# Optimization experiments

Hardware: AMD Instinct MI355X
Metric: run time of the kernel (lower is better)

## Reference

```python
import jax, jax.numpy as jnp
import numpy as np

N_Q = 32   # query window / partition increment
N_K = 128  # key window length
H = 8      # heads


def _ln(x, w=None, b=None, eps=1e-5):
    m = jnp.mean(x, axis=-1, keepdims=True)
    v = jnp.var(x, axis=-1, keepdims=True)
    y = (x - m) * jax.lax.rsqrt(v + eps)
    if w is not None:
        y = y * w
    if b is not None:
        y = y + b
    return y


def setup_inputs() -> dict:
    key = jax.random.key(0)
    ks = jax.random.split(key, 16)
    B, N, C, CP = 1, 2048, 128, 16
    sc = 1.0 / np.sqrt(C)
    inp = {
        "x": jax.random.normal(ks[0], (B, N, C), jnp.float32),
        "s": jax.random.normal(ks[1], (B, N, C), jnp.float32),
        "pair": jax.random.normal(ks[2], (B, N, N, CP), jnp.float32),
        "adaln_s_w": jnp.ones((C,), jnp.float32),
        "adaln_gate_w": jax.random.normal(ks[3], (C, C), jnp.float32) * sc,
        "adaln_gate_b": jnp.zeros((C,), jnp.float32),
        "adaln_skip_w": jax.random.normal(ks[4], (C, C), jnp.float32) * sc,
        "q_w": jax.random.normal(ks[5], (C, C), jnp.float32) * sc,
        "q_b": jnp.zeros((C,), jnp.float32),
        "k_w": jax.random.normal(ks[6], (C, C), jnp.float32) * sc,
        "v_w": jax.random.normal(ks[7], (C, C), jnp.float32) * sc,
        "pair_ln_w": jnp.ones((CP,), jnp.float32),
        "pair_ln_b": jnp.zeros((CP,), jnp.float32),
        "pair_proj_w": jax.random.normal(ks[8], (CP, H), jnp.float32) * 0.25,
        "gate_w": jax.random.normal(ks[9], (C, C), jnp.float32) * sc,
        "attn_proj_w": jax.random.normal(ks[10], (C, C), jnp.float32) * sc,
        "out_w": jax.random.normal(ks[11], (C, C), jnp.float32) * sc,
        "out_b": jnp.full((C,), -2.0, jnp.float32),
    }
    return inp


def reference(x, s, pair, adaln_s_w, adaln_gate_w, adaln_gate_b, adaln_skip_w,
              q_w, q_b, k_w, v_w, pair_ln_w, pair_ln_b, pair_proj_w,
              gate_w, attn_proj_w, out_w, out_b):
    B, N, C = x.shape
    nb = N // N_Q          # number of local blocks
    pad = (N_K - N_Q) // 2  # 48: zero halo on each side
    hd = C // H

    # AdaLN: LN(a) no affine; LN(s) scale-only; gate + skip from s
    a = _ln(x)
    sn = _ln(s, adaln_s_w)
    a = jax.nn.sigmoid(sn @ adaln_gate_w + adaln_gate_b) * a + sn @ adaln_skip_w

    q = a @ q_w + q_b
    k = a @ k_w
    v = a @ v_w

    # local windows: window i covers padded[32i : 32i+128]
    idx = N_Q * jnp.arange(nb)[:, None] + jnp.arange(N_K)[None, :]  # [nb, N_K]

    def window(t):  # [B,N,C] -> [B,nb,N_K,C] with zero-padded edges
        tp = jnp.pad(t, ((0, 0), (pad, pad), (0, 0)))
        return tp[:, idx]

    qb = q.reshape(B, nb, N_Q, H, hd).transpose(0, 3, 1, 2, 4)        # [B,H,nb,NQ,hd]
    kb = window(k).reshape(B, nb, N_K, H, hd).transpose(0, 3, 1, 2, 4)
    vb = window(v).reshape(B, nb, N_K, H, hd).transpose(0, 3, 1, 2, 4)

    # pair bias -> local blocks [B,H,nb,NQ,NK]
    pb = _ln(pair, pair_ln_w, pair_ln_b) @ pair_proj_w                # [B,N,N,H]
    pb = pb.reshape(B, nb, N_Q, N, H)
    pb = jnp.pad(pb, ((0, 0), (0, 0), (0, 0), (pad, pad), (0, 0)))
    pb = jnp.take_along_axis(pb, idx[None, :, None, :, None], axis=3)  # [B,nb,NQ,NK,H]
    bias = pb.transpose(0, 4, 1, 2, 3)

    logits = jnp.einsum('bhnqd,bhnkd->bhnqk', qb, kb) / jnp.sqrt(jnp.float32(hd)) + bias
    attn = jax.nn.softmax(logits, axis=-1)
    o = jnp.einsum('bhnqk,bhnkd->bhnqd', attn, vb)
    o = o.transpose(0, 2, 3, 1, 4).reshape(B, N, C)

    g = jax.nn.sigmoid(o @ gate_w) * o
    out = g @ attn_proj_w
    out = jax.nn.sigmoid(out @ out_w + out_b) * out
    return out
```

## Files before the change

kernel.cpp:

```cpp
#include <hip/hip_runtime.h>
#include <math.h>

#define NTOK 2048
#define CDIM 128
#define HHEADS 8
#define HDIM 16
#define NQW 32
#define NKW 128
#define PADW 48
#define CPD 16
#define BT 8

__device__ __forceinline__ float sigmoid_(float z){ return 1.0f/(1.0f+__expf(-z)); }
__device__ __forceinline__ float rdlane(float v, int l){
    return __int_as_float(__builtin_amdgcn_readlane(__float_as_int(v), l));
}

__global__ __launch_bounds__(512, 4) void k_front(
    const float* __restrict__ x, const float* __restrict__ s,
    const float* __restrict__ s_w,
    const float* __restrict__ gate_w, const float* __restrict__ gate_b,
    const float* __restrict__ skip_w,
    const float* __restrict__ q_w, const float* __restrict__ q_b,
    const float* __restrict__ k_w, const float* __restrict__ v_w,
    const float* __restrict__ pair, const float* __restrict__ pln_w,
    const float* __restrict__ pln_b, const float* __restrict__ pproj,
    float* __restrict__ qo, float* __restrict__ ko, float* __restrict__ vo,
    float* __restrict__ bias)
{
    __shared__ float act_t[CDIM][10];
    __shared__ float sn_t[CDIM][10];
    __shared__ float part[8][2][BT][CDIM];
    const int tid = threadIdx.x;
    const int bid = blockIdx.x;

    if (bid >= NTOK/BT) {
        #pragma unroll
        for (int rep = 0; rep < 2; ++rep) {
            const int idx = (bid - NTOK/BT) * 1024 + rep*512 + tid;
            const int qg = idx >> 7;
            const int j  = idx & 127;
            const int ib = qg >> 5;
            const int qr = qg & 31;
            const int kg = (ib << 5) - PADW + j;
            float outh[HHEADS] = {0,0,0,0,0,0,0,0};
            if (kg >= 0 && kg < NTOK) {
                const float* p = pair + ((size_t)qg * NTOK + kg) * CPD;
                float buf[CPD];
                float sum = 0.f, ssq = 0.f;
                #pragma unroll
                for (int c = 0; c < CPD; c += 4) {
                    const float4 t4 = *(const float4*)(p + c);
                    buf[c+0]=t4.x; buf[c+1]=t4.y; buf[c+2]=t4.z; buf[c+3]=t4.w;
                    sum += t4.x+t4.y+t4.z+t4.w;
                    ssq += t4.x*t4.x+t4.y*t4.y+t4.z*t4.z+t4.w*t4.w;
                }
                const float m  = sum * (1.0f/CPD);
                const float vr = ssq * (1.0f/CPD) - m*m;
                const float rs = rsqrtf(vr + 1e-5f);
                #pragma unroll
                for (int c = 0; c < CPD; ++c) {
                    const float y = (buf[c]-m)*rs*pln_w[c] + pln_b[c];
                    #pragma unroll
                    for (int h = 0; h < HHEADS; ++h)
                        outh[h] = fmaf(y, pproj[c*HHEADS+h], outh[h]);
                }
            }
            float* bb = bias + ((size_t)(ib*HHEADS)*NQW + qr)*NKW + j;
            #pragma unroll
            for (int h = 0; h < HHEADS; ++h)
                bb[(size_t)h*NQW*NKW] = outh[h];
        }
        return;
    }

    const int tok0 = bid * BT;
    const int w = tid >> 6;
    const int L = tid & 63;

    {
        const float2 xv = *(const float2*)(x + (size_t)(tok0+w)*CDIM + 2*L);
        const float2 yv = *(const float2*)(s + (size_t)(tok0+w)*CDIM + 2*L);
        float sx = xv.x+xv.y, sxx = xv.x*xv.x+xv.y*xv.y;
        float sy = yv.x+yv.y, syy = yv.x*yv.x+yv.y*yv.y;
        #pragma unroll
        for (int m = 1; m < 64; m <<= 1) {
            sx  += __shfl_xor(sx,  m, 64);
            sxx += __shfl_xor(sxx, m, 64);
            sy  += __shfl_xor(sy,  m, 64);
            syy += __shfl_xor(syy, m, 64);
        }
        const float inv = 1.0f/128.0f;
        const float mx = sx*inv, vx = sxx*inv - mx*mx;
        const float my = sy*inv, vy = syy*inv - my*my;
        const float rx = rsqrtf(vx+1e-5f), ry = rsqrtf(vy+1e-5f);
        const float2 swv = *(const float2*)(s_w + 2*L);
        act_t[2*L][w]   = (xv.x-mx)*rx;
        act_t[2*L+1][w] = (xv.y-mx)*rx;
        sn_t[2*L][w]    = (yv.x-my)*ry*swv.x;
        sn_t[2*L+1][w]  = (yv.y-my)*ry*swv.y;
    }
    __syncthreads();

    const int i0 = w * 16;
    float snr0 = sn_t[i0 + (L>>3)][L&7];
    float snr1 = sn_t[i0 + 8 + (L>>3)][L&7];

    float ag[8][2] = {{0}}, as_[8][2] = {{0}};
    #pragma unroll
    for (int ii = 0; ii < 16; ++ii) {
        const float2 wg  = *(const float2*)(gate_w + (size_t)(i0+ii)*CDIM + 2*L);
        const float2 wsk = *(const float2*)(skip_w + (size_t)(i0+ii)*CDIM + 2*L);
        #pragma unroll
        for (int t = 0; t < 8; ++t) {
            const int v = ii*8 + t;
            const float a = rdlane((v < 64) ? snr0 : snr1, v & 63);
            ag[t][0]  = fmaf(a, wg.x,  ag[t][0]);
            ag[t][1]  = fmaf(a, wg.y,  ag[t][1]);
            as_[t][0] = fmaf(a, wsk.x, as_[t][0]);
            as_[t][1] = fmaf(a, wsk.y, as_[t][1]);
        }
    }
    #pragma unroll
    for (int t = 0; t < 8; ++t) {
        *(float2*)&part[w][0][t][2*L] = make_float2(ag[t][0],  ag[t][1]);
        *(float2*)&part[w][1][t][2*L] = make_float2(as_[t][0], as_[t][1]);
    }
    __syncthreads();

    const int j  = tid & 127;
    const int tq = tid >> 7;
    {
        float zg[2] = {0,0}, zs[2] = {0,0};
        #pragma unroll
        for (int ww = 0; ww < 8; ++ww) {
            #pragma unroll
            for (int tt = 0; tt < 2; ++tt) {
                zg[tt] += part[ww][0][2*tq+tt][j];
                zs[tt] += part[ww][1][2*tq+tt][j];
            }
        }
        const float gb = gate_b[j];
        const float2 av = *(const float2*)&act_t[j][2*tq];
        const float a2x = sigmoid_(zg[0]+gb)*av.x + zs[0];
        const float a2y = sigmoid_(zg[1]+gb)*av.y + zs[1];
        *(float2*)&sn_t[j][2*tq] = make_float2(a2x, a2y);
    }
    __syncthreads();

    float ar0 = sn_t[i0 + (L>>3)][L&7];
    float ar1 = sn_t[i0 + 8 + (L>>3)][L&7];
    float aq[8][2] = {{0}}, ak[8][2] = {{0}}, avv[8][2] = {{0}};
    #pragma unroll
    for (int ii = 0; ii < 16; ++ii) {
        const float2 wq = *(const float2*)(q_w + (size_t)(i0+ii)*CDIM + 2*L);
        const float2 wk = *(const float2*)(k_w + (size_t)(i0+ii)*CDIM + 2*L);
        const float2 wv = *(const float2*)(v_w + (size_t)(i0+ii)*CDIM + 2*L);
        #pragma unroll
        for (int t = 0; t < 8; ++t) {
            const int v = ii*8 + t;
            const float a = rdlane((v < 64) ? ar0 : ar1, v & 63);
            aq[t][0]  = fmaf(a, wq.x, aq[t][0]);
            aq[t][1]  = fmaf(a, wq.y, aq[t][1]);
            ak[t][0]  = fmaf(a, wk.x, ak[t][0]);
            ak[t][1]  = fmaf(a, wk.y, ak[t][1]);
            avv[t][0] = fmaf(a, wv.x, avv[t][0]);
            avv[t][1] = fmaf(a, wv.y, avv[t][1]);
        }
    }
    #pragma unroll
    for (int t = 0; t < 8; ++t) {
        *(float2*)&part[w][0][t][2*L] = make_float2(aq[t][0], aq[t][1]);
        *(float2*)&part[w][1][t][2*L] = make_float2(ak[t][0], ak[t][1]);
    }
    __syncthreads();
    {
        float zq[2] = {0,0}, zk[2] = {0,0};
        #pragma unroll
        for (int ww = 0; ww < 8; ++ww) {
            #pragma unroll
            for (int tt = 0; tt < 2; ++tt) {
                zq[tt] += part[ww][0][2*tq+tt][j];
                zk[tt] += part[ww][1][2*tq+tt][j];
            }
        }
        const float qbj = q_b[j];
        #pragma unroll
        for (int tt = 0; tt < 2; ++tt) {
            const size_t row = (size_t)(tok0 + 2*tq + tt)*CDIM + j;
            qo[row] = zq[tt] + qbj;
            ko[row] = zk[tt];
        }
    }
    __syncthreads();
    #pragma unroll
    for (int t = 0; t < 8; ++t)
        *(float2*)&part[w][0][t][2*L] = make_float2(avv[t][0], avv[t][1]);
    __syncthreads();
    {
        float zv[2] = {0,0};
        #pragma unroll
        for (int ww = 0; ww < 8; ++ww) {
            #pragma unroll
            for (int tt = 0; tt < 2; ++tt)
                zv[tt] += part[ww][0][2*tq+tt][j];
        }
        #pragma unroll
        for (int tt = 0; tt < 2; ++tt)
            vo[(size_t)(tok0 + 2*tq + tt)*CDIM + j] = zv[tt];
    }
}

__global__ __launch_bounds__(256) void k_attn(
    const float* __restrict__ qi, const float* __restrict__ ki,
    const float* __restrict__ vi, const float* __restrict__ bias,
    float* __restrict__ o)
{
    __shared__ float khs[NKW*20];
    __shared__ float vhs[NKW*20];
    const int ib = blockIdx.x;
    const int h  = blockIdx.y;
    const int t  = threadIdx.x;

    {
        const int jr  = t >> 1;
        const int d08 = (t & 1) * 8;
        const int kg  = ib*NQW - PADW + jr;
        float4 k0 = {0,0,0,0}, k1 = {0,0,0,0};
        float4 v0 = {0,0,0,0}, v1 = {0,0,0,0};
        if (kg >= 0 && kg < NTOK) {
            const float* sk = ki + (size_t)kg*CDIM + h*HDIM + d08;
            const float* sv = vi + (size_t)kg*CDIM + h*HDIM + d08;
            k0 = *(const float4*)sk;  k1 = *(const float4*)(sk+4);
            v0 = *(const float4*)sv;  v1 = *(const float4*)(sv+4);
        }
        *(float4*)&khs[jr*20 + d08]     = k0;
        *(float4*)&khs[jr*20 + d08 + 4] = k1;
        *(float4*)&vhs[jr*20 + d08]     = v0;
        *(float4*)&vhs[jr*20 + d08 + 4] = v1;
    }
    __syncthreads();

    const int rp = t >> 4;
    const int ln = t & 15;
    const int q0 = 2*rp;

    float4 qv[2][4];
    #pragma unroll
    for (int i = 0; i < 2; ++i) {
        const float4* qp = (const float4*)(qi + (size_t)(ib*NQW + q0 + i)*CDIM + h*HDIM);
        #pragma unroll
        for (int dq = 0; dq < 4; ++dq) qv[i][dq] = qp[dq];
    }

    const float* br = bias + ((size_t)(ib*HHEADS + h)*NQW + q0)*NKW;
    float p[2][8];
    #pragma unroll
    for (int m2 = 0; m2 < 8; ++m2) {
        const int k = ln + 16*m2;
        const float4 c0 = *(const float4*)&khs[k*20];
        const float4 c1 = *(const float4*)&khs[k*20 + 4];
        const float4 c2 = *(const float4*)&khs[k*20 + 8];
        const float4 c3 = *(const float4*)&khs[k*20 + 12];
        #pragma unroll
        for (int i = 0; i < 2; ++i) {
            float sdot = qv[i][0].x*c0.x;
            sdot = fmaf(qv[i][0].y, c0.y, sdot);
            sdot = fmaf(qv[i][0].z, c0.z, sdot);
            sdot = fmaf(qv[i][0].w, c0.w, sdot);
            sdot = fmaf(qv[i][1].x, c1.x, sdot);
            sdot = fmaf(qv[i][1].y, c1.y, sdot);
            sdot = fmaf(qv[i][1].z, c1.z, sdot);
            sdot = fmaf(qv[i][1].w, c1.w, sdot);
            sdot = fmaf(qv[i][2].x, c2.x, sdot);
            sdot = fmaf(qv[i][2].y, c2.y, sdot);
            sdot = fmaf(qv[i][2].z, c2.z, sdot);
            sdot = fmaf(qv[i][2].w, c2.w, sdot);
            sdot = fmaf(qv[i][3].x, c3.x, sdot);
            sdot = fmaf(qv[i][3].y, c3.y, sdot);
            sdot = fmaf(qv[i][3].z, c3.z, sdot);
            sdot = fmaf(qv[i][3].w, c3.w, sdot);
            p[i][m2] = sdot*0.25f + br[(size_t)i*NKW + k];
        }
    }

    float smv[2];
    #pragma unroll
    for (int i = 0; i < 2; ++i) {
        float mx = p[i][0];
        #pragma unroll
        for (int m2 = 1; m2 < 8; ++m2) mx = fmaxf(mx, p[i][m2]);
        mx = fmaxf(mx, __shfl_xor(mx, 1, 64));
        mx = fmaxf(mx, __shfl_xor(mx, 2, 64));
        mx = fmaxf(mx, __shfl_xor(mx, 4, 64));
        mx = fmaxf(mx, __shfl_xor(mx, 8, 64));
        float sm = 0.f;
        #pragma unroll
        for (int m2 = 0; m2 < 8; ++m2) { p[i][m2] = __expf(p[i][m2]-mx); sm += p[i][m2]; }
        sm += __shfl_xor(sm, 1, 64);
        sm += __shfl_xor(sm, 2, 64);
        sm += __shfl_xor(sm, 4, 64);
        sm += __shfl_xor(sm, 8, 64);
        smv[i] = sm;
    }

    float ov0[16], ov1[16];
    #pragma unroll
    for (int d = 0; d < 16; ++d) { ov0[d] = 0.f; ov1[d] = 0.f; }
    #pragma unroll
    for (int m2 = 0; m2 < 8; ++m2) {
        const int k = ln + 16*m2;
        const float4 a = *(const float4*)&vhs[k*20];
        const float4 b = *(const float4*)&vhs[k*20 + 4];
        const float4 c = *(const float4*)&vhs[k*20 + 8];
        const float4 d4 = *(const float4*)&vhs[k*20 + 12];
        const float p0 = p[0][m2], p1 = p[1][m2];
        ov0[0] = fmaf(p0, a.x, ov0[0]);  ov1[0] = fmaf(p1, a.x, ov1[0]);
        ov0[1] = fmaf(p0, a.y, ov0[1]);  ov1[1] = fmaf(p1, a.y, ov1[1]);
        ov0[2] = fmaf(p0, a.z, ov0[2]);  ov1[2] = fmaf(p1, a.z, ov1[2]);
        ov0[3] = fmaf(p0, a.w, ov0[3]);  ov1[3] = fmaf(p1, a.w, ov1[3]);
        ov0[4] = fmaf(p0, b.x, ov0[4]);  ov1[4] = fmaf(p1, b.x, ov1[4]);
        ov0[5] = fmaf(p0, b.y, ov0[5]);  ov1[5] = fmaf(p1, b.y, ov1[5]);
        ov0[6] = fmaf(p0, b.z, ov0[6]);  ov1[6] = fmaf(p1, b.z, ov1[6]);
        ov0[7] = fmaf(p0, b.w, ov0[7]);  ov1[7] = fmaf(p1, b.w, ov1[7]);
        ov0[8] = fmaf(p0, c.x, ov0[8]);  ov1[8] = fmaf(p1, c.x, ov1[8]);
        ov0[9] = fmaf(p0, c.y, ov0[9]);  ov1[9] = fmaf(p1, c.y, ov1[9]);
        ov0[10]= fmaf(p0, c.z, ov0[10]); ov1[10]= fmaf(p1, c.z, ov1[10]);
        ov0[11]= fmaf(p0, c.w, ov0[11]); ov1[11]= fmaf(p1, c.w, ov1[11]);
        ov0[12]= fmaf(p0, d4.x, ov0[12]); ov1[12]= fmaf(p1, d4.x, ov1[12]);
        ov0[13]= fmaf(p0, d4.y, ov0[13]); ov1[13]= fmaf(p1, d4.y, ov1[13]);
        ov0[14]= fmaf(p0, d4.z, ov0[14]); ov1[14]= fmaf(p1, d4.z, ov1[14]);
        ov0[15]= fmaf(p0, d4.w, ov0[15]); ov1[15]= fmaf(p1, d4.w, ov1[15]);
    }

    float e0, e1;
    {
        float r8a[8], r8b[8];
        #pragma unroll
        for (int j2 = 0; j2 < 8; ++j2) {
            const float lo0 = ov0[j2]   + __shfl_xor(ov0[j2],   8, 64);
            const float hi0 = ov0[j2+8] + __shfl_xor(ov0[j2+8], 8, 64);
            r8a[j2] = (ln & 8) ? hi0 : lo0;
            const float lo1 = ov1[j2]   + __shfl_xor(ov1[j2],   8, 64);
            const float hi1 = ov1[j2+8] + __shfl_xor(ov1[j2+8], 8, 64);
            r8b[j2] = (ln & 8) ? hi1 : lo1;
        }
        float r4a[4], r4b[4];
        #pragma unroll
        for (int j2 = 0; j2 < 4; ++j2) {
            const float lo0 = r8a[j2]   + __shfl_xor(r8a[j2],   4, 64);
            const float hi0 = r8a[j2+4] + __shfl_xor(r8a[j2+4], 4, 64);
            r4a[j2] = (ln & 4) ? hi0 : lo0;
            const float lo1 = r8b[j2]   + __shfl_xor(r8b[j2],   4, 64);
            const float hi1 = r8b[j2+4] + __shfl_xor(r8b[j2+4], 4, 64);
            r4b[j2] = (ln & 4) ? hi1 : lo1;
        }
        float r2a[2], r2b[2];
        #pragma unroll
        for (int j2 = 0; j2 < 2; ++j2) {
            const float lo0 = r4a[j2]   + __shfl_xor(r4a[j2],   2, 64);
            const float hi0 = r4a[j2+2] + __shfl_xor(r4a[j2+2], 2, 64);
            r2a[j2] = (ln & 2) ? hi0 : lo0;
            const float lo1 = r4b[j2]   + __shfl_xor(r4b[j2],   2, 64);
            const float hi1 = r4b[j2+2] + __shfl_xor(r4b[j2+2], 2, 64);
            r2b[j2] = (ln & 2) ? hi1 : lo1;
        }
        {
            const float lo0 = r2a[0] + __shfl_xor(r2a[0], 1, 64);
            const float hi0 = r2a[1] + __shfl_xor(r2a[1], 1, 64);
            e0 = (ln & 1) ? hi0 : lo0;
            const float lo1 = r2b[0] + __shfl_xor(r2b[0], 1, 64);
            const float hi1 = r2b[1] + __shfl_xor(r2b[1], 1, 64);
            e1 = (ln & 1) ? hi1 : lo1;
        }
    }

    float* dst = o + (size_t)(ib*NQW + q0)*CDIM + h*HDIM + ln;
    dst[0]    = e0 * (1.0f / smv[0]);
    dst[CDIM] = e1 * (1.0f / smv[1]);
}

__global__ __launch_bounds__(512) void k_back(
    const float* __restrict__ oin, const float* __restrict__ gate_w,
    const float* __restrict__ proj_w, const float* __restrict__ out_w,
    const float* __restrict__ out_b, float* __restrict__ out)
{
    __shared__ float b0_t[CDIM][10];
    __shared__ float b1_t[CDIM][10];
    __shared__ float part[8][BT][CDIM];
    const int tid = threadIdx.x;
    const int tok0 = blockIdx.x * BT;
    const int w = tid >> 6, L = tid & 63;
    const int j = tid & 127, tq = tid >> 7;

    {
        const float2 ov = *(const float2*)(oin + (size_t)tok0*CDIM + 2*tid);
        const int e = 2*tid, c = e & 127, t = e >> 7;
        b0_t[c][t]   = ov.x;
        b0_t[c+1][t] = ov.y;
    }
    __syncthreads();

    const int i0 = w * 16;

    {
        const float r0 = b0_t[i0 + (L>>3)][L&7];
        const float r1 = b0_t[i0 + 8 + (L>>3)][L&7];
        float acc[8][2] = {{0}};
        #pragma unroll
        for (int ii = 0; ii < 16; ++ii) {
            const float2 wv = *(const float2*)(gate_w + (size_t)(i0+ii)*CDIM + 2*L);
            #pragma unroll
            for (int t = 0; t < 8; ++t) {
                const int v = ii*8 + t;
                const float a = rdlane((v < 64) ? r0 : r1, v & 63);
                acc[t][0] = fmaf(a, wv.x, acc[t][0]);
                acc[t][1] = fmaf(a, wv.y, acc[t][1]);
            }
        }
        #pragma unroll
        for (int t = 0; t < 8; ++t)
            *(float2*)&part[w][t][2*L] = make_float2(acc[t][0], acc[t][1]);
    }
    __syncthreads();
    {
        float z[2] = {0,0};
        #pragma unroll
        for (int ww = 0; ww < 8; ++ww) {
            z[0] += part[ww][2*tq][j];
            z[1] += part[ww][2*tq+1][j];
        }
        const float2 ov = *(const float2*)&b0_t[j][2*tq];
        *(float2*)&b1_t[j][2*tq] = make_float2(sigmoid_(z[0])*ov.x, sigmoid_(z[1])*ov.y);
    }
    __syncthreads();

    {
        const float r0 = b1_t[i0 + (L>>3)][L&7];
        const float r1 = b1_t[i0 + 8 + (L>>3)][L&7];
        float acc[8][2] = {{0}};
        #pragma unroll
        for (int ii = 0; ii < 16; ++ii) {
            const float2 wv = *(const float2*)(proj_w + (size_t)(i0+ii)*CDIM + 2*L);
            #pragma unroll
            for (int t = 0; t < 8; ++t) {
                const int v = ii*8 + t;
                const float a = rdlane((v < 64) ? r0 : r1, v & 63);
                acc[t][0] = fmaf(a, wv.x, acc[t][0]);
                acc[t][1] = fmaf(a, wv.y, acc[t][1]);
            }
        }
        #pragma unroll
        for (int t = 0; t < 8; ++t)
            *(float2*)&part[w][t][2*L] = make_float2(acc[t][0], acc[t][1]);
    }
    __syncthreads();
    float t2v[2];
    {
        float z[2] = {0,0};
        #pragma unroll
        for (int ww = 0; ww < 8; ++ww) {
            z[0] += part[ww][2*tq][j];
            z[1] += part[ww][2*tq+1][j];
        }
        t2v[0] = z[0]; t2v[1] = z[1];
        *(float2*)&b0_t[j][2*tq] = make_float2(z[0], z[1]);
    }
    __syncthreads();

    {
        const float r0 = b0_t[i0 + (L>>3)][L&7];
        const float r1 = b0_t[i0 + 8 + (L>>3)][L&7];
        float acc[8][2] = {{0}};
        #pragma unroll
        for (int ii = 0; ii < 16; ++ii) {
            const float2 wv = *(const float2*)(out_w + (size_t)(i0+ii)*CDIM + 2*L);
            #pragma unroll
            for (int t = 0; t < 8; ++t) {
                const int v = ii*8 + t;
                const float a = rdlane((v < 64) ? r0 : r1, v & 63);
                acc[t][0] = fmaf(a, wv.x, acc[t][0]);
                acc[t][1] = fmaf(a, wv.y, acc[t][1]);
            }
        }
        #pragma unroll
        for (int t = 0; t < 8; ++t)
            *(float2*)&part[w][t][2*L] = make_float2(acc[t][0], acc[t][1]);
    }
    __syncthreads();
    {
        float z[2] = {0,0};
        #pragma unroll
        for (int ww = 0; ww < 8; ++ww) {
            z[0] += part[ww][2*tq][j];
            z[1] += part[ww][2*tq+1][j];
        }
        const float ob = out_b[j];
        out[(size_t)(tok0 + 2*tq)*CDIM + j]     = sigmoid_(z[0]+ob)*t2v[0];
        out[(size_t)(tok0 + 2*tq + 1)*CDIM + j] = sigmoid_(z[1]+ob)*t2v[1];
    }
}

extern "C" void kernel_launch(void* const* d_in, const int* in_sizes, int n_in,
                              void* d_out, int out_size, void* d_ws, size_t ws_size,
                              hipStream_t stream) {
    (void)in_sizes; (void)n_in; (void)out_size; (void)ws_size;
    const float* x           = (const float*)d_in[0];
    const float* s           = (const float*)d_in[1];
    const float* pair        = (const float*)d_in[2];
    const float* adaln_s_w   = (const float*)d_in[3];
    const float* adaln_gate_w= (const float*)d_in[4];
    const float* adaln_gate_b= (const float*)d_in[5];
    const float* adaln_skip_w= (const float*)d_in[6];
    const float* q_w         = (const float*)d_in[7];
    const float* q_b         = (const float*)d_in[8];
    const float* k_w         = (const float*)d_in[9];
    const float* v_w         = (const float*)d_in[10];
    const float* pair_ln_w   = (const float*)d_in[11];
    const float* pair_ln_b   = (const float*)d_in[12];
    const float* pair_proj_w = (const float*)d_in[13];
    const float* gate_w      = (const float*)d_in[14];
    const float* attn_proj_w = (const float*)d_in[15];
    const float* out_w       = (const float*)d_in[16];
    const float* out_b       = (const float*)d_in[17];
    float* out = (float*)d_out;

    float* ws = (float*)d_ws;
    float* q_ws    = ws;
    float* k_ws    = ws + 262144;
    float* v_ws    = ws + 524288;
    float* o_ws    = ws + 786432;
    float* bias_ws = ws + 1048576;

    k_front<<<NTOK/BT + (NTOK*NKW)/1024, 512, 0, stream>>>(
        x, s, adaln_s_w, adaln_gate_w, adaln_gate_b, adaln_skip_w,
        q_w, q_b, k_w, v_w, pair, pair_ln_w, pair_ln_b, pair_proj_w,
        q_ws, k_ws, v_ws, bias_ws);
    k_attn<<<dim3(NTOK/NQW, HHEADS), 256, 0, stream>>>(q_ws, k_ws, v_ws, bias_ws, o_ws);
    k_back<<<NTOK/BT, 512, 0, stream>>>(o_ws, gate_w, attn_proj_w, out_w, out_b, out);
}
```

Baseline: 34.58 us.

## Fuse three kernels into one persistent kernel with grid barriers

Merges the front (AdaLN/QKV/pair bias), attention and back (gating/projections) kernels into a single 512-block kernel that separates phases with atomic-counter grid barriers, with a memset to reset the counters. Shared memory is pooled into one array and reused across phases. The aim is to remove launch gaps and tail effects between kernels. In exchange it relies on all 512 blocks being co-resident (otherwise it deadlocks), adds spin-wait barrier cost, and leaves half the threads idle in the attention phase.

New measurement: 127.3 us. +268.1%, slower.

```diff
diff --git a/kernel.cpp b/kernel.cpp
--- a/kernel.cpp
+++ b/kernel.cpp
@@ -10,13 +10,27 @@
 #define PADW 48
 #define CPD 16
 #define BT 8
+#define NBLK 512u
 
 __device__ __forceinline__ float sigmoid_(float z){ return 1.0f/(1.0f+__expf(-z)); }
 __device__ __forceinline__ float rdlane(float v, int l){
     return __int_as_float(__builtin_amdgcn_readlane(__float_as_int(v), l));
 }
 
-__global__ __launch_bounds__(512, 4) void k_front(
+__device__ __forceinline__ void grid_barrier(unsigned* bar, unsigned nb) {
+    __syncthreads();
+    if (threadIdx.x == 0) {
+        __threadfence();
+        atomicAdd(bar, 1u);
+        while (__hip_atomic_load(bar, __ATOMIC_RELAXED, __HIP_MEMORY_SCOPE_AGENT) < nb) {
+            __builtin_amdgcn_s_sleep(2);
+        }
+        __threadfence();
+    }
+    __syncthreads();
+}
+
+__device__ __forceinline__ void front_phase(
     const float* __restrict__ x, const float* __restrict__ s,
     const float* __restrict__ s_w,
     const float* __restrict__ gate_w, const float* __restrict__ gate_b,
@@ -26,14 +40,10 @@
     const float* __restrict__ pair, const float* __restrict__ pln_w,
     const float* __restrict__ pln_b, const float* __restrict__ pproj,
     float* __restrict__ qo, float* __restrict__ ko, float* __restrict__ vo,
-    float* __restrict__ bias)
+    float* __restrict__ bias,
+    float* __restrict__ act_t, float* __restrict__ sn_t, float* __restrict__ part,
+    int bid, int tid)
 {
-    __shared__ float act_t[CDIM][10];
-    __shared__ float sn_t[CDIM][10];
-    __shared__ float part[8][2][BT][CDIM];
-    const int tid = threadIdx.x;
-    const int bid = blockIdx.x;
-
     if (bid >= NTOK/BT) {
         #pragma unroll
         for (int rep = 0; rep < 2; ++rep) {
@@ -95,16 +105,16 @@
         const float my = sy*inv, vy = syy*inv - my*my;
         const float rx = rsqrtf(vx+1e-5f), ry = rsqrtf(vy+1e-5f);
         const float2 swv = *(const float2*)(s_w + 2*L);
-        act_t[2*L][w]   = (xv.x-mx)*rx;
-        act_t[2*L+1][w] = (xv.y-mx)*rx;
-        sn_t[2*L][w]    = (yv.x-my)*ry*swv.x;
-        sn_t[2*L+1][w]  = (yv.y-my)*ry*swv.y;
+        act_t[(2*L)*10 + w]   = (xv.x-mx)*rx;
+        act_t[(2*L+1)*10 + w] = (xv.y-mx)*rx;
+        sn_t[(2*L)*10 + w]    = (yv.x-my)*ry*swv.x;
+        sn_t[(2*L+1)*10 + w]  = (yv.y-my)*ry*swv.y;
     }
     __syncthreads();
 
     const int i0 = w * 16;
-    float snr0 = sn_t[i0 + (L>>3)][L&7];
-    float snr1 = sn_t[i0 + 8 + (L>>3)][L&7];
+    float snr0 = sn_t[(i0 + (L>>3))*10 + (L&7)];
+    float snr1 = sn_t[(i0 + 8 + (L>>3))*10 + (L&7)];
 
     float ag[8][2] = {{0}}, as_[8][2] = {{0}};
     #pragma unroll
@@ -123,8 +133,8 @@
     }
     #pragma unroll
     for (int t = 0; t < 8; ++t) {
-        *(float2*)&part[w][0][t][2*L] = make_float2(ag[t][0],  ag[t][1]);
-        *(float2*)&part[w][1][t][2*L] = make_float2(as_[t][0], as_[t][1]);
+        *(float2*)&part[((w*2+0)*8+t)*128 + 2*L] = make_float2(ag[t][0],  ag[t][1]);
+        *(float2*)&part[((w*2+1)*8+t)*128 + 2*L] = make_float2(as_[t][0], as_[t][1]);
     }
     __syncthreads();
 
@@ -136,20 +146,20 @@
         for (int ww = 0; ww < 8; ++ww) {
             #pragma unroll
             for (int tt = 0; tt < 2; ++tt) {
-                zg[tt] += part[ww][0][2*tq+tt][j];
-                zs[tt] += part[ww][1][2*tq+tt][j];
+                zg[tt] += part[((ww*2+0)*8 + 2*tq+tt)*128 + j];
+                zs[tt] += part[((ww*2+1)*8 + 2*tq+tt)*128 + j];
             }
         }
         const float gb = gate_b[j];
-        const float2 av = *(const float2*)&act_t[j][2*tq];
+        const float2 av = *(const float2*)&act_t[j*10 + 2*tq];
         const float a2x = sigmoid_(zg[0]+gb)*av.x + zs[0];
         const float a2y = sigmoid_(zg[1]+gb)*av.y + zs[1];
-        *(float2*)&sn_t[j][2*tq] = make_float2(a2x, a2y);
-    }
-    __syncthreads();
-
-    float ar0 = sn_t[i0 + (L>>3)][L&7];
-    float ar1 = sn_t[i0 + 8 + (L>>3)][L&7];
+        *(float2*)&sn_t[j*10 + 2*tq] = make_float2(a2x, a2y);
+    }
+    __syncthreads();
+
+    float ar0 = sn_t[(i0 + (L>>3))*10 + (L&7)];
+    float ar1 = sn_t[(i0 + 8 + (L>>3))*10 + (L&7)];
     float aq[8][2] = {{0}}, ak[8][2] = {{0}}, avv[8][2] = {{0}};
     #pragma unroll
     for (int ii = 0; ii < 16; ++ii) {
@@ -170,8 +180,8 @@
     }
     #pragma unroll
     for (int t = 0; t < 8; ++t) {
-        *(float2*)&part[w][0][t][2*L] = make_float2(aq[t][0], aq[t][1]);
-        *(float2*)&part[w][1][t][2*L] = make_float2(ak[t][0], ak[t][1]);
+        *(float2*)&part[((w*2+0)*8+t)*128 + 2*L] = make_float2(aq[t][0], aq[t][1]);
+        *(float2*)&part[((w*2+1)*8+t)*128 + 2*L] = make_float2(ak[t][0], ak[t][1]);
     }
     __syncthreads();
     {
@@ -180,8 +190,8 @@
         for (int ww = 0; ww < 8; ++ww) {
             #pragma unroll
             for (int tt = 0; tt < 2; ++tt) {
-                zq[tt] += part[ww][0][2*tq+tt][j];
-                zk[tt] += part[ww][1][2*tq+tt][j];
+                zq[tt] += part[((ww*2+0)*8 + 2*tq+tt)*128 + j];
+                zk[tt] += part[((ww*2+1)*8 + 2*tq+tt)*128 + j];
             }
         }
         const float qbj = q_b[j];
@@ -195,7 +205,7 @@
     __syncthreads();
     #pragma unroll
     for (int t = 0; t < 8; ++t)
-        *(float2*)&part[w][0][t][2*L] = make_float2(avv[t][0], avv[t][1]);
+        *(float2*)&part[((w*2+0)*8+t)*128 + 2*L] = make_float2(avv[t][0], avv[t][1]);
     __syncthreads();
     {
         float zv[2] = {0,0};
@@ -203,7 +213,7 @@
         for (int ww = 0; ww < 8; ++ww) {
             #pragma unroll
             for (int tt = 0; tt < 2; ++tt)
-                zv[tt] += part[ww][0][2*tq+tt][j];
+                zv[tt] += part[((ww*2+0)*8 + 2*tq+tt)*128 + j];
         }
         #pragma unroll
         for (int tt = 0; tt < 2; ++tt)
@@ -211,18 +221,14 @@
     }
 }
 
-__global__ __launch_bounds__(256) void k_attn(
+__device__ __forceinline__ void attn_phase(
     const float* __restrict__ qi, const float* __restrict__ ki,
     const float* __restrict__ vi, const float* __restrict__ bias,
-    float* __restrict__ o)
+    float* __restrict__ o,
+    float* __restrict__ khs, float* __restrict__ vhs,
+    int ib, int h, int t, bool act)
 {
-    __shared__ float khs[NKW*20];
-    __shared__ float vhs[NKW*20];
-    const int ib = blockIdx.x;
-    const int h  = blockIdx.y;
-    const int t  = threadIdx.x;
-
-    {
+    if (act) {
         const int jr  = t >> 1;
         const int d08 = (t & 1) * 8;
         const int kg  = ib*NQW - PADW + jr;
@@ -240,6 +246,7 @@
         *(float4*)&vhs[jr*20 + d08 + 4] = v1;
     }
     __syncthreads();
+    if (!act) return;
 
     const int rp = t >> 4;
     const int ln = t & 15;
@@ -380,32 +387,29 @@
     dst[CDIM] = e1 * (1.0f / smv[1]);
 }
 
-__global__ __launch_bounds__(512) void k_back(
+__device__ __forceinline__ void back_phase(
     const float* __restrict__ oin, const float* __restrict__ gate_w,
     const float* __restrict__ proj_w, const float* __restrict__ out_w,
-    const float* __restrict__ out_b, float* __restrict__ out)
+    const float* __restrict__ out_b, float* __restrict__ out,
+    float* __restrict__ b0_t, float* __restrict__ b1_t, float* __restrict__ part,
+    int tok0, int tid)
 {
-    __shared__ float b0_t[CDIM][10];
-    __shared__ float b1_t[CDIM][10];
-    __shared__ float part[8][BT][CDIM];
-    const int tid = threadIdx.x;
-    const int tok0 = blockIdx.x * BT;
     const int w = tid >> 6, L = tid & 63;
     const int j = tid & 127, tq = tid >> 7;
 
     {
         const float2 ov = *(const float2*)(oin + (size_t)tok0*CDIM + 2*tid);
         const int e = 2*tid, c = e & 127, t = e >> 7;
-        b0_t[c][t]   = ov.x;
-        b0_t[c+1][t] = ov.y;
+        b0_t[c*10 + t]     = ov.x;
+        b0_t[(c+1)*10 + t] = ov.y;
     }
     __syncthreads();
 
     const int i0 = w * 16;
 
     {
-        const float r0 = b0_t[i0 + (L>>3)][L&7];
-        const float r1 = b0_t[i0 + 8 + (L>>3)][L&7];
+        const float r0 = b0_t[(i0 + (L>>3))*10 + (L&7)];
+        const float r1 = b0_t[(i0 + 8 + (L>>3))*10 + (L&7)];
         float acc[8][2] = {{0}};
         #pragma unroll
         for (int ii = 0; ii < 16; ++ii) {
@@ -420,24 +424,24 @@
         }
         #pragma unroll
         for (int t = 0; t < 8; ++t)
-            *(float2*)&part[w][t][2*L] = make_float2(acc[t][0], acc[t][1]);
+            *(float2*)&part[(w*8+t)*128 + 2*L] = make_float2(acc[t][0], acc[t][1]);
     }
     __syncthreads();
     {
         float z[2] = {0,0};
         #pragma unroll
         for (int ww = 0; ww < 8; ++ww) {
-            z[0] += part[ww][2*tq][j];
-            z[1] += part[ww][2*tq+1][j];
-        }
-        const float2 ov = *(const float2*)&b0_t[j][2*tq];
-        *(float2*)&b1_t[j][2*tq] = make_float2(sigmoid_(z[0])*ov.x, sigmoid_(z[1])*ov.y);
-    }
-    __syncthreads();
-
-    {
-        const float r0 = b1_t[i0 + (L>>3)][L&7];
-        const float r1 = b1_t[i0 + 8 + (L>>3)][L&7];
+            z[0] += part[(ww*8 + 2*tq)*128 + j];
+            z[1] += part[(ww*8 + 2*tq+1)*128 + j];
+        }
+        const float2 ov = *(const float2*)&b0_t[j*10 + 2*tq];
+        *(float2*)&b1_t[j*10 + 2*tq] = make_float2(sigmoid_(z[0])*ov.x, sigmoid_(z[1])*ov.y);
+    }
+    __syncthreads();
+
+    {
+        const float r0 = b1_t[(i0 + (L>>3))*10 + (L&7)];
+        const float r1 = b1_t[(i0 + 8 + (L>>3))*10 + (L&7)];
         float acc[8][2] = {{0}};
         #pragma unroll
         for (int ii = 0; ii < 16; ++ii) {
@@ -452,7 +456,7 @@
         }
         #pragma unroll
         for (int t = 0; t < 8; ++t)
-            *(float2*)&part[w][t][2*L] = make_float2(acc[t][0], acc[t][1]);
+            *(float2*)&part[(w*8+t)*128 + 2*L] = make_float2(acc[t][0], acc[t][1]);
     }
     __syncthreads();
     float t2v[2];
@@ -460,17 +464,17 @@
         float z[2] = {0,0};
         #pragma unroll
         for (int ww = 0; ww < 8; ++ww) {
-            z[0] += part[ww][2*tq][j];
-            z[1] += part[ww][2*tq+1][j];
+            z[0] += part[(ww*8 + 2*tq)*128 + j];
+            z[1] += part[(ww*8 + 2*tq+1)*128 + j];
         }
         t2v[0] = z[0]; t2v[1] = z[1];
-        *(float2*)&b0_t[j][2*tq] = make_float2(z[0], z[1]);
-    }
-    __syncthreads();
-
-    {
-        const float r0 = b0_t[i0 + (L>>3)][L&7];
-        const float r1 = b0_t[i0 + 8 + (L>>3)][L&7];
+        *(float2*)&b0_t[j*10 + 2*tq] = make_float2(z[0], z[1]);
+    }
+    __syncthreads();
+
+    {
+        const float r0 = b0_t[(i0 + (L>>3))*10 + (L&7)];
+        const float r1 = b0_t[(i0 + 8 + (L>>3))*10 + (L&7)];
         float acc[8][2] = {{0}};
         #pragma unroll
         for (int ii = 0; ii < 16; ++ii) {
@@ -485,20 +489,56 @@
         }
         #pragma unroll
         for (int t = 0; t < 8; ++t)
-            *(float2*)&part[w][t][2*L] = make_float2(acc[t][0], acc[t][1]);
+            *(float2*)&part[(w*8+t)*128 + 2*L] = make_float2(acc[t][0], acc[t][1]);
     }
     __syncthreads();
     {
         float z[2] = {0,0};
         #pragma unroll
         for (int ww = 0; ww < 8; ++ww) {
-            z[0] += part[ww][2*tq][j];
-            z[1] += part[ww][2*tq+1][j];
+            z[0] += part[(ww*8 + 2*tq)*128 + j];
+            z[1] += part[(ww*8 + 2*tq+1)*128 + j];
         }
         const float ob = out_b[j];
         out[(size_t)(tok0 + 2*tq)*CDIM + j]     = sigmoid_(z[0]+ob)*t2v[0];
         out[(size_t)(tok0 + 2*tq + 1)*CDIM + j] = sigmoid_(z[1]+ob)*t2v[1];
     }
+}
+
+__global__ __launch_bounds__(512, 4) void k_all(
+    const float* __restrict__ x, const float* __restrict__ s,
+    const float* __restrict__ s_w,
+    const float* __restrict__ gate_w, const float* __restrict__ gate_b,
+    const float* __restrict__ skip_w,
+    const float* __restrict__ q_w, const float* __restrict__ q_b,
+    const float* __restrict__ k_w, const float* __restrict__ v_w,
+    const float* __restrict__ pair, const float* __restrict__ pln_w,
+    const float* __restrict__ pln_b, const float* __restrict__ pproj,
+    const float* __restrict__ ogate_w, const float* __restrict__ oproj_w,
+    const float* __restrict__ oout_w, const float* __restrict__ oout_b,
+    float* __restrict__ qo, float* __restrict__ ko, float* __restrict__ vo,
+    float* __restrict__ oo, float* __restrict__ bias, float* __restrict__ out,
+    unsigned* __restrict__ bar)
+{
+    __shared__ float lds[18944];
+    const int tid = threadIdx.x;
+    const int bid = blockIdx.x;
+
+    front_phase(x, s, s_w, gate_w, gate_b, skip_w, q_w, q_b, k_w, v_w,
+                pair, pln_w, pln_b, pproj, qo, ko, vo, bias,
+                lds, lds + 1280, lds + 2560, bid, tid);
+
+    grid_barrier(bar + 0, NBLK);
+
+    attn_phase(qo, ko, vo, bias, oo,
+               lds, lds + 2560,
+               bid >> 3, bid & 7, tid & 255, tid < 256);
+
+    grid_barrier(bar + 1, NBLK);
+
+    if (bid < NTOK/BT)
+        back_phase(oo, ogate_w, oproj_w, oout_w, oout_b, out,
+                   lds, lds + 1280, lds + 2560, bid * BT, tid);
 }
 
 extern "C" void kernel_launch(void* const* d_in, const int* in_sizes, int n_in,
@@ -531,11 +571,12 @@
     float* v_ws    = ws + 524288;
     float* o_ws    = ws + 786432;
     float* bias_ws = ws + 1048576;
-
-    k_front<<<NTOK/BT + (NTOK*NKW)/1024, 512, 0, stream>>>(
+    unsigned* bar  = (unsigned*)(ws + 4194304);
+
+    hipMemsetAsync(bar, 0, 2*sizeof(unsigned), stream);
+    k_all<<<NBLK, 512, 0, stream>>>(
         x, s, adaln_s_w, adaln_gate_w, adaln_gate_b, adaln_skip_w,
         q_w, q_b, k_w, v_w, pair, pair_ln_w, pair_ln_b, pair_proj_w,
-        q_ws, k_ws, v_ws, bias_ws);
-    k_attn<<<dim3(NTOK/NQW, HHEADS), 256, 0, stream>>>(q_ws, k_ws, v_ws, bias_ws, o_ws);
-    k_back<<<NTOK/BT, 512, 0, stream>>>(o_ws, gate_w, attn_proj_w, out_w, out_b, out);
-}
+        gate_w, attn_proj_w, out_w, out_b,
+        q_ws, k_ws, v_ws, o_ws, bias_ws, out, bar);
+}
```
